# Kernel optimization log

Hardware: AMD Instinct MI355X
Metric: run time of the kernel (lower is better)

Reference implementation:

```python
import jax, jax.numpy as jnp
import numpy as np

B, MN, GN, ME, GE = 1, 40962, 65160, 327660, 163848
MEMB = EEMB = 256
H1, H2 = 512, 64
EPS = 1e-5


def setup_inputs() -> dict:
    key = jax.random.key(0)
    ks = jax.random.split(key, 16)
    s = 0.05
    return {
        "gx": jax.random.normal(ks[0], (B, GN, MEMB), jnp.float32),
        "mx": jax.random.normal(ks[1], (B, MN, MEMB), jnp.float32),
        "me_i": jax.random.randint(ks[2], (2, ME), 0, MN),
        "me_x": jax.random.normal(ks[3], (B, ME, EEMB), jnp.float32),
        "g2me_i": jax.random.randint(ks[4], (2, GE), 0, MN),
        "g2me_x": jax.random.normal(ks[5], (B, GE, EEMB), jnp.float32),
        "m2ge_i": jax.random.randint(ks[6], (2, GE), 0, MN),
        "m2ge_x": jax.random.normal(ks[7], (B, GE, EEMB), jnp.float32),
        # learned params (Linear stored as [in, out]; y = x @ W + b, math-equivalent to torch)
        "W1": jax.random.normal(ks[8], (2 * MEMB + EEMB, H1), jnp.float32) * s,
        "b1": jnp.zeros((H1,), jnp.float32),
        "W2": jax.random.normal(ks[9], (H1, H2), jnp.float32) * s,
        "b2": jnp.zeros((H2,), jnp.float32),
        "W3": jax.random.normal(ks[10], (H2, EEMB), jnp.float32) * s,
        "b3": jnp.zeros((EEMB,), jnp.float32),
        # LayerNorm([m_enum, eemb]) -> elementwise affine over last two dims
        "ln_w": jnp.ones((ME, EEMB), jnp.float32),
        "ln_b": jnp.zeros((ME, EEMB), jnp.float32),
    }


def reference(gx, mx, me_i, me_x, g2me_i, g2me_x, m2ge_i, m2ge_x,
              W1, b1, W2, b2, W3, b3, ln_w, ln_b):
    row, col = me_i[0], me_i[1]
    # gather sender/receiver mesh-node features per edge: [B, ME, 2*MEMB+EEMB]
    h = jnp.concatenate([mx[:, row], mx[:, col], me_x], axis=-1)
    h = jax.nn.silu(h @ W1 + b1)
    h = jax.nn.silu(h @ W2 + b2)
    h = h @ W3 + b3
    # LayerNorm over the last TWO dims (m_enum, eemb), as nn.LayerNorm([m_enum, eemb])
    mean = jnp.mean(h, axis=(-2, -1), keepdims=True)
    var = jnp.var(h, axis=(-2, -1), keepdims=True)
    h = (h - mean) * jax.lax.rsqrt(var + EPS) * ln_w + ln_b
    me_x_new = me_x + h
    return (gx, mx, me_i, me_x_new, g2me_i, g2me_x, m2ge_i, m2ge_x)
```

## Files before the change

### kernel.cpp

```cpp
#include <hip/hip_runtime.h>
#include <hip/hip_bf16.h>

typedef unsigned short u16;
typedef unsigned int u32;
typedef __attribute__((ext_vector_type(8))) short bfrag8;
typedef __attribute__((ext_vector_type(4))) float f32x4;

#define ME_N 327660
#define MN_N 40962
#define MEMB_N 256
#define H1_N 512
#define H2_N 64
#define EEMB_N 256
#define LN_EPS 1e-5f
#define NBLK 5120

static __device__ __forceinline__ u16 f2bf(float f) {
  __hip_bfloat16 h = __float2bfloat16(f);
  return *reinterpret_cast<u16*>(&h);
}
static __device__ __forceinline__ float bf2f(u16 u) {
  union { u32 i; float f; } x; x.i = ((u32)u) << 16; return x.f;
}
static __device__ __forceinline__ u32 pack2(float a, float b) {
  return (u32)f2bf(a) | ((u32)f2bf(b) << 16);
}
static __device__ __forceinline__ float silu_f(float x) {
  return x / (1.0f + __expf(-x));
}
static __device__ __forceinline__ void gload_lds16(const void* g, void* l) {
  __builtin_amdgcn_global_load_lds(
      (const __attribute__((address_space(1))) void*)g,
      (__attribute__((address_space(3))) void*)l, 16, 0, 0);
}

__global__ void i2f_kernel(const int* __restrict__ src, float* __restrict__ dst, int n) {
  int i = blockIdx.x * 256 + threadIdx.x;
  if (i < n) dst[i] = (float)src[i];
}

__global__ void bfconv_kernel(const float* __restrict__ src, u16* __restrict__ dst, int n) {
  int i = (blockIdx.x * 256 + threadIdx.x) * 8;
  if (i >= n) return;
  float4 v0 = reinterpret_cast<const float4*>(src + i)[0];
  float4 v1 = reinterpret_cast<const float4*>(src + i)[1];
  uint4 q;
  q.x = pack2(v0.x, v0.y); q.y = pack2(v0.z, v0.w);
  q.z = pack2(v1.x, v1.y); q.w = pack2(v1.z, v1.w);
  *reinterpret_cast<uint4*>(dst + i) = q;
}

__global__ void wconv1_kernel(const float* __restrict__ src, u16* __restrict__ dst) {
  int i = blockIdx.x * 256 + threadIdx.x;
  if (i >= 512 * 768) return;
  int e   = i & 7;
  int l16 = (i >> 3) & 15;
  int k4  = (i >> 7) & 3;
  int ks  = (i >> 9) & 1;
  int rest = i >> 10;
  int kc = rest % 12;
  int J  = rest / 12;
  int n = J * 16 + l16;
  int k = kc * 64 + ks * 32 + k4 * 8 + e;
  dst[i] = f2bf(src[(size_t)k * 512 + n]);
}

__global__ void wconv_kernel(const float* __restrict__ src, u16* __restrict__ dst,
                             int K, int N) {
  int i = blockIdx.x * 256 + threadIdx.x;
  if (i >= K * N) return;
  int n = i / K;
  int k = i - n * K;
  dst[i] = f2bf(src[(size_t)k * N + n]);
}

__launch_bounds__(512, 4)
__global__ void gemm_fused_kernel(const u16* __restrict__ mxb, const int* __restrict__ me_i,
                                  const float* __restrict__ me_x,
                                  const u16* __restrict__ w1f, const float* __restrict__ b1,
                                  const u16* __restrict__ w2t, const float* __restrict__ b2,
                                  const u16* __restrict__ w3t, const float* __restrict__ b3,
                                  u16* __restrict__ h3, float* __restrict__ partials) {
  __shared__ u16 S[16384];
  __shared__ float red[16];

  const int t = threadIdx.x;
  const int m0 = blockIdx.x * 64;
  const int lane = t & 63;
  const int w = t >> 6;
  const int l16 = lane & 15;
  const int k4 = lane >> 4;
  const int h7 = l16 & 7;

  const int r_st = t >> 3;
  const int g_st = t & 7;
  const int gsw = ((g_st ^ (r_st & 7)) * 8);
  const int mg = min(m0 + r_st, ME_N - 1);
  const u16* rowr = mxb + (size_t)me_i[mg] * MEMB_N;
  const u16* rowc = mxb + (size_t)me_i[ME_N + mg] * MEMB_N;
  const float* pe = me_x + (size_t)mg * EEMB_N;

  const f32x4 zero = {0.f, 0.f, 0.f, 0.f};
  f32x4 acc[4][4];
#pragma unroll
  for (int jj = 0; jj < 4; ++jj)
#pragma unroll
    for (int i = 0; i < 4; ++i) acc[jj][i] = zero;

  auto stage_A = [&](int kcn) {
    const int buf = (kcn & 1) * 4096;
    if (kcn < 8) {
      const u16* src = (kcn < 4 ? rowr : rowc) + (kcn & 3) * 64 + gsw;
      gload_lds16(src, S + buf + w * 512);
    } else {
      const float4* p4 = reinterpret_cast<const float4*>(pe + (kcn - 8) * 64 + g_st * 8);
      float4 v0 = p4[0], v1 = p4[1];
      uint4 q;
      q.x = pack2(v0.x, v0.y); q.y = pack2(v0.z, v0.w);
      q.z = pack2(v1.x, v1.y); q.w = pack2(v1.z, v1.w);
      *reinterpret_cast<uint4*>(S + buf + r_st * 64 + gsw) = q;
    }
  };

  stage_A(0);
  __syncthreads();

  for (int kc = 0; kc < 12; ++kc) {
    if (kc < 11) stage_A(kc + 1);
    const u16* ab = S + (kc & 1) * 4096;
    const u16* wb = w1f + (size_t)w * 12288 + (size_t)kc * 1024 + k4 * 128 + l16 * 8;
#pragma unroll
    for (int ks = 0; ks < 2; ++ks) {
      bfrag8 a[4];
#pragma unroll
      for (int i = 0; i < 4; ++i)
        a[i] = *reinterpret_cast<const bfrag8*>(
            &ab[(i * 16 + l16) * 64 + (((ks * 4 + k4) ^ h7) * 8)]);
#pragma unroll
      for (int jj = 0; jj < 4; ++jj) {
        bfrag8 bf = *reinterpret_cast<const bfrag8*>(wb + (size_t)jj * 98304 + ks * 512);
#pragma unroll
        for (int i = 0; i < 4; ++i)
          acc[jj][i] = __builtin_amdgcn_mfma_f32_16x16x32_bf16(bf, a[i], acc[jj][i], 0, 0, 0);
      }
    }
    __syncthreads();
  }

  const int kh = w >> 2;
  const int g4 = w & 3;
  const int n2 = g4 * 16 + l16;
  bfrag8 w2f8[8];
#pragma unroll
  for (int ksl = 0; ksl < 8; ++ksl)
    w2f8[ksl] = *reinterpret_cast<const bfrag8*>(
        w2t + (size_t)n2 * 512 + kh * 256 + ksl * 32 + k4 * 8);

  f32x4 acc2p[4];
#pragma unroll
  for (int i = 0; i < 4; ++i) acc2p[i] = zero;

#pragma unroll
  for (int h = 0; h < 2; ++h) {
#pragma unroll
    for (int jr = 0; jr < 2; ++jr) {
      const int jj = 2 * h + jr;
      const float4 bq = *reinterpret_cast<const float4*>(b1 + jj * 128 + w * 16 + k4 * 4);
      const int col = jr * 128 + w * 16 + k4 * 4;
      const int grp = col >> 3, off = col & 7;
#pragma unroll
      for (int i = 0; i < 4; ++i) {
        float x0 = silu_f(acc[jj][i][0] + bq.x);
        float x1 = silu_f(acc[jj][i][1] + bq.y);
        float x2 = silu_f(acc[jj][i][2] + bq.z);
        float x3 = silu_f(acc[jj][i][3] + bq.w);
        uint2 pq = make_uint2(pack2(x0, x1), pack2(x2, x3));
        *reinterpret_cast<uint2*>(&S[(i * 16 + l16) * 256 + ((grp ^ h7) * 8 + off)]) = pq;
      }
    }
    __syncthreads();
    if (kh == h) {
#pragma unroll
      for (int ksl = 0; ksl < 8; ++ksl) {
#pragma unroll
        for (int i = 0; i < 4; ++i) {
          bfrag8 a2 = *reinterpret_cast<const bfrag8*>(
              &S[(i * 16 + l16) * 256 + (((ksl * 4 + k4) ^ h7) * 8)]);
          acc2p[i] = __builtin_amdgcn_mfma_f32_16x16x32_bf16(w2f8[ksl], a2, acc2p[i], 0, 0, 0);
        }
      }
    }
    __syncthreads();
  }

  float* LDSf = reinterpret_cast<float*>(S);
  u16* h2T = S + 12288;
  if (kh == 1) {
#pragma unroll
    for (int i = 0; i < 4; ++i)
      *reinterpret_cast<f32x4*>(&LDSf[((g4 * 4 + i) * 64 + lane) * 4]) = acc2p[i];
  }
  __syncthreads();
  if (kh == 0) {
    const float4 b2q = *reinterpret_cast<const float4*>(b2 + g4 * 16 + k4 * 4);
    const int col = g4 * 16 + k4 * 4;
    const int grp = col >> 3, off = col & 7;
#pragma unroll
    for (int i = 0; i < 4; ++i) {
      f32x4 o = *reinterpret_cast<f32x4*>(&LDSf[((g4 * 4 + i) * 64 + lane) * 4]);
      float x0 = silu_f(acc2p[i][0] + o[0] + b2q.x);
      float x1 = silu_f(acc2p[i][1] + o[1] + b2q.y);
      float x2 = silu_f(acc2p[i][2] + o[2] + b2q.z);
      float x3 = silu_f(acc2p[i][3] + o[3] + b2q.w);
      uint2 pq = make_uint2(pack2(x0, x1), pack2(x2, x3));
      *reinterpret_cast<uint2*>(&h2T[(i * 16 + l16) * 64 + ((grp ^ h7) * 8 + off)]) = pq;
    }
  }
  __syncthreads();

  bfrag8 a3[2][4];
#pragma unroll
  for (int ks = 0; ks < 2; ++ks)
#pragma unroll
    for (int i = 0; i < 4; ++i)
      a3[ks][i] = *reinterpret_cast<const bfrag8*>(
          &h2T[(i * 16 + l16) * 64 + (((ks * 4 + k4) ^ h7) * 8)]);
  bfrag8 w3f[2][2];
#pragma unroll
  for (int j = 0; j < 2; ++j)
#pragma unroll
    for (int ks = 0; ks < 2; ++ks)
      w3f[j][ks] = *reinterpret_cast<const bfrag8*>(
          w3t + (size_t)(w * 32 + j * 16 + l16) * 64 + ks * 32 + k4 * 8);
  __syncthreads();

  f32x4 acc3[2][4];
#pragma unroll
  for (int j = 0; j < 2; ++j)
#pragma unroll
    for (int i = 0; i < 4; ++i) acc3[j][i] = zero;
#pragma unroll
  for (int ks = 0; ks < 2; ++ks)
#pragma unroll
    for (int j = 0; j < 2; ++j)
#pragma unroll
      for (int i = 0; i < 4; ++i)
        acc3[j][i] = __builtin_amdgcn_mfma_f32_16x16x32_bf16(w3f[j][ks], a3[ks][i], acc3[j][i], 0, 0, 0);

  float lsum = 0.f, lsq = 0.f;
#pragma unroll
  for (int j = 0; j < 2; ++j) {
    const float4 b3q = *reinterpret_cast<const float4*>(b3 + w * 32 + j * 16 + k4 * 4);
    const int col = w * 32 + j * 16 + k4 * 4;
    const int grp = col >> 3, off = col & 7;
#pragma unroll
    for (int i = 0; i < 4; ++i) {
      float x0 = acc3[j][i][0] + b3q.x;
      float x1 = acc3[j][i][1] + b3q.y;
      float x2 = acc3[j][i][2] + b3q.z;
      float x3 = acc3[j][i][3] + b3q.w;
      if (m0 + i * 16 + l16 < ME_N) {
        lsum += (x0 + x1) + (x2 + x3);
        lsq += x0 * x0 + x1 * x1 + x2 * x2 + x3 * x3;
      }
      uint2 pq = make_uint2(pack2(x0, x1), pack2(x2, x3));
      *reinterpret_cast<uint2*>(&S[(i * 16 + l16) * 256 + ((grp ^ h7) * 8 + off)]) = pq;
    }
  }
#pragma unroll
  for (int o = 32; o > 0; o >>= 1) {
    lsum += __shfl_down(lsum, o, 64);
    lsq  += __shfl_down(lsq, o, 64);
  }
  if (lane == 0) { red[w] = lsum; red[8 + w] = lsq; }
  __syncthreads();

  {
    u16* dst = h3 + (size_t)(m0 + r_st) * EEMB_N;
#pragma unroll
    for (int q = 0; q < 4; ++q) {
      const int G = q * 8 + g_st;
      uint4 v = *reinterpret_cast<const uint4*>(&S[r_st * 256 + ((G ^ (r_st & 7)) * 8)]);
      *reinterpret_cast<uint4*>(dst + G * 8) = v;
    }
  }
  if (t == 0) {
    float s1 = 0.f, s2 = 0.f;
#pragma unroll
    for (int q = 0; q < 8; ++q) { s1 += red[q]; s2 += red[8 + q]; }
    partials[2 * blockIdx.x] = s1;
    partials[2 * blockIdx.x + 1] = s2;
  }
}

__global__ void reduce_kernel(const float* __restrict__ partials, int n,
                              float* __restrict__ stats) {
  __shared__ float s1[256], s2[256];
  float a = 0.f, b = 0.f;
  for (int i = threadIdx.x; i < n; i += 256) { a += partials[2 * i]; b += partials[2 * i + 1]; }
  s1[threadIdx.x] = a; s2[threadIdx.x] = b;
  __syncthreads();
  for (int off = 128; off > 0; off >>= 1) {
    if ((int)threadIdx.x < off) {
      s1[threadIdx.x] += s1[threadIdx.x + off];
      s2[threadIdx.x] += s2[threadIdx.x + off];
    }
    __syncthreads();
  }
  if (threadIdx.x == 0) {
    double cnt = (double)ME_N * (double)EEMB_N;
    double mean = (double)s1[0] / cnt;
    double var = (double)s2[0] / cnt - mean * mean;
    stats[0] = (float)mean;
    stats[1] = (float)(1.0 / sqrt(var + (double)LN_EPS));
  }
}

__launch_bounds__(256)
__global__ void final_kernel(const u16* __restrict__ h3, const float* __restrict__ me_x,
                             const float* __restrict__ ln_w, const float* __restrict__ ln_b,
                             const float* __restrict__ stats, float* __restrict__ out) {
  const size_t total = (size_t)ME_N * EEMB_N;
  size_t i = ((size_t)blockIdx.x * 256 + threadIdx.x) * 8;
  if (i >= total) return;
  const float mean = stats[0], inv = stats[1];
  uint4 hv = *reinterpret_cast<const uint4*>(h3 + i);
  float h[8];
  h[0] = bf2f((u16)(hv.x & 0xffff)); h[1] = bf2f((u16)(hv.x >> 16));
  h[2] = bf2f((u16)(hv.y & 0xffff)); h[3] = bf2f((u16)(hv.y >> 16));
  h[4] = bf2f((u16)(hv.z & 0xffff)); h[5] = bf2f((u16)(hv.z >> 16));
  h[6] = bf2f((u16)(hv.w & 0xffff)); h[7] = bf2f((u16)(hv.w >> 16));
  float4 m0 = reinterpret_cast<const float4*>(me_x + i)[0];
  float4 m1 = reinterpret_cast<const float4*>(me_x + i)[1];
  float4 w0 = reinterpret_cast<const float4*>(ln_w + i)[0];
  float4 w1 = reinterpret_cast<const float4*>(ln_w + i)[1];
  float4 c0 = reinterpret_cast<const float4*>(ln_b + i)[0];
  float4 c1 = reinterpret_cast<const float4*>(ln_b + i)[1];
  float4 o0, o1;
  o0.x = m0.x + (h[0] - mean) * inv * w0.x + c0.x;
  o0.y = m0.y + (h[1] - mean) * inv * w0.y + c0.y;
  o0.z = m0.z + (h[2] - mean) * inv * w0.z + c0.z;
  o0.w = m0.w + (h[3] - mean) * inv * w0.w + c0.w;
  o1.x = m1.x + (h[4] - mean) * inv * w1.x + c1.x;
  o1.y = m1.y + (h[5] - mean) * inv * w1.y + c1.y;
  o1.z = m1.z + (h[6] - mean) * inv * w1.z + c1.z;
  o1.w = m1.w + (h[7] - mean) * inv * w1.w + c1.w;
  reinterpret_cast<float4*>(out + i)[0] = o0;
  reinterpret_cast<float4*>(out + i)[1] = o1;
}

extern "C" void kernel_launch(void* const* d_in, const int* in_sizes, int n_in,
                              void* d_out, int out_size, void* d_ws, size_t ws_size,
                              hipStream_t stream) {
  const float* mx   = (const float*)d_in[1];
  const int*   me_i = (const int*)d_in[2];
  const float* me_x = (const float*)d_in[3];
  const float* W1 = (const float*)d_in[8];
  const float* b1 = (const float*)d_in[9];
  const float* W2 = (const float*)d_in[10];
  const float* b2 = (const float*)d_in[11];
  const float* W3 = (const float*)d_in[12];
  const float* b3 = (const float*)d_in[13];
  const float* ln_w = (const float*)d_in[14];
  const float* ln_b = (const float*)d_in[15];

  char* ws = (char*)d_ws;
  u16* w1f = (u16*)(ws + 0);
  u16* w2t = (u16*)(ws + 786432);
  u16* w3t = (u16*)(ws + 851968);
  u16* mxb = (u16*)(ws + 884736);
  u16* h3  = (u16*)(ws + 21857280);
  float* partials = (float*)(ws + 189629440);
  float* stats    = (float*)(ws + 189670400);

  size_t off[8]; size_t a = 0;
  for (int i = 0; i < 8; ++i) { off[i] = a; a += (size_t)in_sizes[i]; }

  for (int i = 0; i < 8; ++i) {
    if (i == 3) continue;
    if (i == 2 || i == 4 || i == 6) {
      int n = in_sizes[i];
      i2f_kernel<<<(n + 255) / 256, 256, 0, stream>>>(
          (const int*)d_in[i], (float*)d_out + off[i], n);
    } else {
      hipMemcpyAsync((char*)d_out + off[i] * 4, d_in[i], (size_t)in_sizes[i] * 4,
                     hipMemcpyDeviceToDevice, stream);
    }
  }

  wconv1_kernel<<<(512 * 768 + 255) / 256, 256, 0, stream>>>(W1, w1f);
  wconv_kernel<<<(512 * 64 + 255) / 256, 256, 0, stream>>>(W2, w2t, 512, 64);
  wconv_kernel<<<(64 * 256 + 255) / 256, 256, 0, stream>>>(W3, w3t, 64, 256);
  {
    int n = MN_N * MEMB_N;
    bfconv_kernel<<<(n / 8 + 255) / 256, 256, 0, stream>>>(mx, mxb, n);
  }

  gemm_fused_kernel<<<NBLK, 512, 0, stream>>>(mxb, me_i, me_x, w1f, b1, w2t, b2,
                                              w3t, b3, h3, partials);
  reduce_kernel<<<1, 256, 0, stream>>>(partials, NBLK, stats);

  const size_t total8 = (size_t)ME_N * EEMB_N / 8;
  final_kernel<<<(int)((total8 + 255) / 256), 256, 0, stream>>>(
      h3, me_x, ln_w, ln_b, stats, (float*)d_out + off[3]);
}
```

Before: 915.5 us.

## Software-pipeline first GEMM with register-prefetched weights and split-barrier DMA waits

Restructures the first-layer K loop so each iteration prefetches all W1 fragments into registers, issues the next A-tile DMA, then waits with explicit vmcnt counts and raw s_barrier instead of full __syncthreads. The me_x fp32 loads are issued before compute and converted and stored after it, so their latency hides behind MFMA work. W2 fragments are now loaded inside the loop rather than kept in registers, and launch bounds drop from 4 to 2 blocks per CU to make room for the extra live registers. This lowers the occupancy floor and relies on hand-tuned waitcnt values being correct.

Measured after the change: 1.122 ms. 1.23x slower.

```diff
diff --git a/kernel.cpp b/kernel.cpp
--- a/kernel.cpp
+++ b/kernel.cpp
@@ -74,7 +74,7 @@
   dst[i] = f2bf(src[(size_t)k * N + n]);
 }
 
-__launch_bounds__(512, 4)
+__launch_bounds__(512, 2)
 __global__ void gemm_fused_kernel(const u16* __restrict__ mxb, const int* __restrict__ me_i,
                                   const float* __restrict__ me_x,
                                   const u16* __restrict__ w1f, const float* __restrict__ b1,
@@ -92,13 +92,12 @@
   const int k4 = lane >> 4;
   const int h7 = l16 & 7;
 
-  const int r_st = t >> 3;
-  const int g_st = t & 7;
-  const int gsw = ((g_st ^ (r_st & 7)) * 8);
+  const int r_st = t >> 3, g_st = t & 7;
+  const int gsw = (g_st ^ (r_st & 7)) * 8;
   const int mg = min(m0 + r_st, ME_N - 1);
   const u16* rowr = mxb + (size_t)me_i[mg] * MEMB_N;
   const u16* rowc = mxb + (size_t)me_i[ME_N + mg] * MEMB_N;
-  const float* pe = me_x + (size_t)mg * EEMB_N;
+  const float* pef = me_x + (size_t)mg * EEMB_N + gsw;
 
   const f32x4 zero = {0.f, 0.f, 0.f, 0.f};
   f32x4 acc[4][4];
@@ -107,28 +106,20 @@
 #pragma unroll
     for (int i = 0; i < 4; ++i) acc[jj][i] = zero;
 
-  auto stage_A = [&](int kcn) {
-    const int buf = (kcn & 1) * 4096;
-    if (kcn < 8) {
-      const u16* src = (kcn < 4 ? rowr : rowc) + (kcn & 3) * 64 + gsw;
-      gload_lds16(src, S + buf + w * 512);
-    } else {
-      const float4* p4 = reinterpret_cast<const float4*>(pe + (kcn - 8) * 64 + g_st * 8);
-      float4 v0 = p4[0], v1 = p4[1];
-      uint4 q;
-      q.x = pack2(v0.x, v0.y); q.y = pack2(v0.z, v0.w);
-      q.z = pack2(v1.x, v1.y); q.w = pack2(v1.z, v1.w);
-      *reinterpret_cast<uint4*>(S + buf + r_st * 64 + gsw) = q;
-    }
+  auto stage_dma = [&](int kcn) {
+    const u16* src = (kcn < 4 ? rowr : rowc) + (kcn & 3) * 64 + gsw;
+    gload_lds16(src, S + (kcn & 1) * 4096 + w * 512);
   };
-
-  stage_A(0);
-  __syncthreads();
-
-  for (int kc = 0; kc < 12; ++kc) {
-    if (kc < 11) stage_A(kc + 1);
+  auto loadB = [&](int kc, bfrag8 (&bfr)[2][4]) {
+    const u16* wbase = w1f + (size_t)w * 12288 + (size_t)kc * 1024 + k4 * 128 + l16 * 8;
+#pragma unroll
+    for (int ks = 0; ks < 2; ++ks)
+#pragma unroll
+      for (int jj = 0; jj < 4; ++jj)
+        bfr[ks][jj] = *reinterpret_cast<const bfrag8*>(wbase + (size_t)jj * 98304 + ks * 512);
+  };
+  auto compute = [&](int kc, const bfrag8 (&bfr)[2][4]) {
     const u16* ab = S + (kc & 1) * 4096;
-    const u16* wb = w1f + (size_t)w * 12288 + (size_t)kc * 1024 + k4 * 128 + l16 * 8;
 #pragma unroll
     for (int ks = 0; ks < 2; ++ks) {
       bfrag8 a[4];
@@ -137,24 +128,63 @@
         a[i] = *reinterpret_cast<const bfrag8*>(
             &ab[(i * 16 + l16) * 64 + (((ks * 4 + k4) ^ h7) * 8)]);
 #pragma unroll
-      for (int jj = 0; jj < 4; ++jj) {
-        bfrag8 bf = *reinterpret_cast<const bfrag8*>(wb + (size_t)jj * 98304 + ks * 512);
+      for (int jj = 0; jj < 4; ++jj)
 #pragma unroll
         for (int i = 0; i < 4; ++i)
-          acc[jj][i] = __builtin_amdgcn_mfma_f32_16x16x32_bf16(bf, a[i], acc[jj][i], 0, 0, 0);
-      }
-    }
-    __syncthreads();
-  }
+          acc[jj][i] = __builtin_amdgcn_mfma_f32_16x16x32_bf16(bfr[ks][jj], a[i], acc[jj][i], 0, 0, 0);
+    }
+  };
+
+  stage_dma(0);
+  for (int kc = 0; kc < 7; ++kc) {
+    bfrag8 bfr[2][4];
+    loadB(kc, bfr);
+    stage_dma(kc + 1);
+    asm volatile("s_waitcnt vmcnt(9)" ::: "memory");
+    __builtin_amdgcn_s_barrier();
+    compute(kc, bfr);
+    __builtin_amdgcn_s_barrier();
+  }
+  float4 fA, fB;
+  {
+    bfrag8 bfr[2][4];
+    loadB(7, bfr);
+    fA = reinterpret_cast<const float4*>(pef)[0];
+    fB = reinterpret_cast<const float4*>(pef)[1];
+    asm volatile("s_waitcnt vmcnt(10)" ::: "memory");
+    __builtin_amdgcn_s_barrier();
+    compute(7, bfr);
+    uint4 q;
+    q.x = pack2(fA.x, fA.y); q.y = pack2(fA.z, fA.w);
+    q.z = pack2(fB.x, fB.y); q.w = pack2(fB.z, fB.w);
+    *reinterpret_cast<uint4*>(S + 0 * 4096 + r_st * 64 + g_st * 8) = q;
+    asm volatile("s_waitcnt lgkmcnt(0)" ::: "memory");
+    __builtin_amdgcn_s_barrier();
+  }
+  for (int kc = 8; kc < 11; ++kc) {
+    bfrag8 bfr[2][4];
+    loadB(kc, bfr);
+    const float* ps = pef + (kc - 7) * 64;
+    fA = reinterpret_cast<const float4*>(ps)[0];
+    fB = reinterpret_cast<const float4*>(ps)[1];
+    compute(kc, bfr);
+    uint4 q;
+    q.x = pack2(fA.x, fA.y); q.y = pack2(fA.z, fA.w);
+    q.z = pack2(fB.x, fB.y); q.w = pack2(fB.z, fB.w);
+    *reinterpret_cast<uint4*>(S + ((kc + 1) & 1) * 4096 + r_st * 64 + g_st * 8) = q;
+    asm volatile("s_waitcnt lgkmcnt(0)" ::: "memory");
+    __builtin_amdgcn_s_barrier();
+  }
+  {
+    bfrag8 bfr[2][4];
+    loadB(11, bfr);
+    compute(11, bfr);
+  }
+  __syncthreads();
 
   const int kh = w >> 2;
   const int g4 = w & 3;
   const int n2 = g4 * 16 + l16;
-  bfrag8 w2f8[8];
-#pragma unroll
-  for (int ksl = 0; ksl < 8; ++ksl)
-    w2f8[ksl] = *reinterpret_cast<const bfrag8*>(
-        w2t + (size_t)n2 * 512 + kh * 256 + ksl * 32 + k4 * 8);
 
   f32x4 acc2p[4];
 #pragma unroll
@@ -182,11 +212,13 @@
     if (kh == h) {
 #pragma unroll
       for (int ksl = 0; ksl < 8; ++ksl) {
+        bfrag8 w2f = *reinterpret_cast<const bfrag8*>(
+            w2t + (size_t)n2 * 512 + kh * 256 + ksl * 32 + k4 * 8);
 #pragma unroll
         for (int i = 0; i < 4; ++i) {
           bfrag8 a2 = *reinterpret_cast<const bfrag8*>(
               &S[(i * 16 + l16) * 256 + (((ksl * 4 + k4) ^ h7) * 8)]);
-          acc2p[i] = __builtin_amdgcn_mfma_f32_16x16x32_bf16(w2f8[ksl], a2, acc2p[i], 0, 0, 0);
+          acc2p[i] = __builtin_amdgcn_mfma_f32_16x16x32_bf16(w2f, a2, acc2p[i], 0, 0, 0);
         }
       }
     }
```
